# Optimization experiments

Measured on AMD Instinct MI355X. Metric: run time of the kernel, lower is better.

## Reference

```python
import jax, jax.numpy as jnp
import numpy as np

B, N, E, S, A, P, T = 512, 65536, 131072, 256, 512, 2, 64


def setup_inputs() -> dict:
    key = jax.random.key(0)
    ks = jax.random.split(key, 40)
    f32 = jnp.float32

    def g(i, shape, s=0.05):
        return jax.random.normal(ks[i], shape, f32) * s

    inp = {
        'nodes': jax.random.normal(ks[0], (N, S), f32),
        'edge_features': jax.random.normal(ks[1], (E, S), f32),
        'edge_source': jax.random.randint(ks[2], (E,), 0, N),
        'edge_dest': jax.random.randint(ks[3], (E,), 0, N),
        'node_owner': jax.random.randint(ks[4], (N,), 0, B),
        'running': jnp.ones((B,), bool),
        'ref_types': jax.random.randint(ks[5], (B,), 0, T),
        # decision aggregator (transform + sigmoid gate)
        'dec_t_W': g(6, (A, S)), 'dec_t_b': g(7, (A,)),
        'dec_g_W': g(8, (A, S)), 'dec_g_b': jnp.ones((A,), f32),
        # init aggregator
        'init_t_W': g(9, (A, S)), 'init_t_b': g(10, (A,)),
        'init_g_W': g(11, (A, S)), 'init_g_b': jnp.ones((A,), f32),
        # node type decision head + embedding
        'ntd_W': g(12, (T + 1, A)), 'ntd_b': g(13, (T + 1,)),
        'nte': g(14, (T, S), 1.0),
        # f_init
        'f1_W': g(15, (S, S)), 'f1_b': g(16, (S,)),
        'f2_W': g(17, (S, A)),
        # propagator params, stacked over P steps (message_size = 2S)
        'mn_W': g(18, (P, 2 * S, S)),
        'mf_W': g(19, (P, 2 * S, S)),
        'ml2_W': g(20, (P, 2 * S, 2 * S)), 'ml2_b': g(21, (P, 2 * S)),
        'gru_Wih': g(22, (P, 3 * S, 2 * S)), 'gru_Whh': g(23, (P, 3 * S, S)),
        'gru_bih': jnp.zeros((P, 3 * S), f32),
        'gru_bhh': jnp.concatenate(
            [jnp.ones((P, S), f32), jnp.zeros((P, 2 * S), f32)], axis=-1),
    }
    return inp


def _aggregate(nodes, fmask, tW, tb, gW, gb):
    # Aggregator.forward: sigmoid gate * linear transform, pooled per graph
    # via dense 0/1 owner-mask matmul (dropout=0 -> identity).
    gates = jax.nn.sigmoid(nodes @ gW.T + gb)
    data = nodes @ tW.T + tb
    return fmask @ (data * gates)  # [B, A]


def reference(nodes, edge_features, edge_source, edge_dest, node_owner,
              running, ref_types,
              dec_t_W, dec_t_b, dec_g_W, dec_g_b,
              init_t_W, init_t_b, init_g_W, init_g_b,
              ntd_W, ntd_b, nte, f1_W, f1_b, f2_W,
              mn_W, mf_W, ml2_W, ml2_b, gru_Wih, gru_Whh, gru_bih, gru_bhh):
    f32 = nodes.dtype
    fmask = (node_owner[None, :] == jnp.arange(B)[:, None]).astype(f32)  # [B,N]
    # Propagator._node_update_mask: owner_masks[running].sum(0) > 0
    upd = (fmask * running[:, None].astype(f32)).sum(0) > 0  # [N]

    for p in range(P):
        ef = edge_features @ mf_W[p].T                 # [E, 2S]
        nf = nodes @ mn_W[p].T                         # [N, 2S]
        msgs = nf[edge_source] + nf[edge_dest] + ef
        msgs = jnp.tanh(msgs) @ ml2_W[p].T + ml2_b[p]  # message_layer_2
        inputs = jnp.zeros((N, 2 * S), f32)
        inputs = inputs.at[edge_dest].add(msgs).at[edge_source].add(msgs)
        # torch GRUCell (gate order r, z, n)
        gi = inputs @ gru_Wih[p].T + gru_bih[p]
        gh = nodes @ gru_Whh[p].T + gru_bhh[p]
        ir, iz, inn = jnp.split(gi, 3, axis=-1)
        hr, hz, hn = jnp.split(gh, 3, axis=-1)
        r = jax.nn.sigmoid(ir + hr)
        z = jax.nn.sigmoid(iz + hz)
        n = jnp.tanh(inn + r * hn)
        new_nodes = (1.0 - z) * n + z * nodes
        nodes = jnp.where(upd[:, None], new_nodes, nodes)

    # node-type decision
    agg = _aggregate(nodes, fmask, dec_t_W, dec_t_b, dec_g_W, dec_g_b)
    logits = agg @ ntd_W.T + ntd_b                      # [B, T+1]

    # training path: remap_pad (no pad chars present) -> ref + 1
    sel = ref_types + 1                                  # in [1, T]
    logp = jax.nn.log_softmax(logits, axis=-1)
    per_ex = -logp[jnp.arange(B), sel]
    loss = jnp.where(running, per_ex, 0.0).mean()

    # new node features for running graphs
    emb = nte[sel - 1]                                   # [B, S]
    init_feats = _aggregate(nodes, fmask, init_t_W, init_t_b,
                            init_g_W, init_g_b)
    new_features = emb @ f1_W.T + f1_b + init_feats @ f2_W.T  # [B, S]
    return logits, new_features, loss
```

## Files before the change

kernel.cpp:

```cpp
#include <hip/hip_runtime.h>
#include <hip/hip_bf16.h>
#include <math.h>

#define BG 512
#define NN 65536
#define EE 131072
#define SD 256
#define AD 512
#define PP 2
#define TD 64

typedef __attribute__((ext_vector_type(8))) short sx8;
typedef __attribute__((ext_vector_type(4))) short sx4;
typedef __attribute__((ext_vector_type(4))) float fx4;

__device__ __forceinline__ float bs2f(short s) {
    union { unsigned u; float f; } x; x.u = ((unsigned)(unsigned short)s) << 16; return x.f;
}
__device__ __forceinline__ short f2bs(float f) {
    union { float f; unsigned u; } x; x.f = f;
    unsigned r = x.u + 0x7fffu + ((x.u >> 16) & 1u);
    return (short)(r >> 16);
}
__device__ __forceinline__ float fast_tanh(float x) {
    float xc = fminf(fmaxf(x, -15.f), 15.f);
    float e = __expf(2.f * xc);
    return __fdividef(e - 1.f, e + 1.f);
}
__device__ __forceinline__ float fast_sigm(float x) {
    float xc = fminf(fmaxf(x, -30.f), 30.f);
    float e = __expf(-xc);
    return __fdividef(1.f, 1.f + e);
}
__device__ __forceinline__ bool run_flag(const void* runv, int idx) {
    const unsigned char* r8 = (const unsigned char*)runv;
    const int* r32 = (const int*)runv;
    return (r8[idx] != 0) || (r32[idx] != 0);
}

__device__ __forceinline__ void gload16(const short* g, short* l) {
    __builtin_amdgcn_global_load_lds(
        (const __attribute__((address_space(1))) void*)g,
        (__attribute__((address_space(3))) void*)l, 16, 0, 0);
}

template<int EPI>
__launch_bounds__(256, 4)
__global__ void gemm_bt(const short* __restrict__ Abp,
                        const short* __restrict__ Wp, const float* __restrict__ bias,
                        short* __restrict__ Cout, float* __restrict__ Fout,
                        const float* __restrict__ bias2,
                        const short* __restrict__ nfp,
                        const int* __restrict__ esrc, const int* __restrict__ edst,
                        int K, int NC, int NT)
{
    __shared__ __align__(16) short sA[2 * 4096];
    __shared__ __align__(16) short sB[2 * 4096];
    const int t = threadIdx.x;
    const int lane = t & 63;
    const int w = t >> 6;

    const int nwg = gridDim.x;
    const int q = nwg >> 3;
    const int wg = (blockIdx.x & 7) * q + (blockIdx.x >> 3);
    const int mt = wg / NT;
    const int nt = wg - mt * NT;
    const int m0 = mt * 128;
    const int n0 = nt * 128;

    const int wm = (w >> 1) * 64;
    const int wn = (w & 1) * 64;
    const int lr = lane & 15;
    const int lg = lane >> 4;

    fx4 acc[4][4];
#pragma unroll
    for (int i = 0; i < 4; i++)
#pragma unroll
        for (int j = 0; j < 4; j++) { fx4 z = {0.f, 0.f, 0.f, 0.f}; acc[i][j] = z; }

    const int r = t >> 2;
    const int cblk = (t & 3) ^ ((r >> 1) & 3);
    const short* gA = Abp + (size_t)(m0 + r) * K + cblk * 8;
    const short* gB = Wp + (size_t)(n0 + r) * K + cblk * 8;
    const size_t rowskip = (size_t)64 * K;

    auto STAGE = [&](int b, int kk) {
        gload16(gA + kk,           sA + b * 4096 + w * 512);
        gload16(gA + kk + rowskip, sA + b * 4096 + 2048 + w * 512);
        gload16(gB + kk,           sB + b * 4096 + w * 512);
        gload16(gB + kk + rowskip, sB + b * 4096 + 2048 + w * 512);
    };

    STAGE(0, 0);
    __syncthreads();
    int buf = 0;
    const int xa = (lr >> 1) & 3;
    for (int kk = 0; kk < K; kk += 32) {
        if (kk + 32 < K) STAGE(buf ^ 1, kk + 32);
        const short* cA = sA + buf * 4096;
        const short* cB = sB + buf * 4096;
        sx8 af[4], bfr[4];
#pragma unroll
        for (int mi = 0; mi < 4; mi++)
            af[mi] = *(const sx8*)(cA + (wm + mi * 16 + lr) * 32 + (lg ^ xa) * 8);
#pragma unroll
        for (int ni = 0; ni < 4; ni++)
            bfr[ni] = *(const sx8*)(cB + (wn + ni * 16 + lr) * 32 + (lg ^ xa) * 8);
#pragma unroll
        for (int mi = 0; mi < 4; mi++)
#pragma unroll
            for (int ni = 0; ni < 4; ni++) {
                if (EPI == 4)
                    acc[mi][ni] = __builtin_amdgcn_mfma_f32_16x16x32_bf16(
                        af[mi], bfr[ni], acc[mi][ni], 0, 0, 0);
                else
                    acc[mi][ni] = __builtin_amdgcn_mfma_f32_16x16x32_bf16(
                        bfr[ni], af[mi], acc[mi][ni], 0, 0, 0);
            }
        __syncthreads();
        buf ^= 1;
    }

    if (EPI == 4) {
#pragma unroll
        for (int mi = 0; mi < 4; mi++) {
#pragma unroll
            for (int rg = 0; rg < 4; rg++) {
                const int m = m0 + wm + mi * 16 + lg * 4 + rg;
#pragma unroll
                for (int ni = 0; ni < 4; ni += 2) {
                    const int rc = (((n0 + wn + ni * 16) >> 5) << 4) + lr;
                    float dv = acc[mi][ni][rg] + bias[rc];
                    float gv = fast_sigm(acc[mi][ni + 1][rg] + bias2[rc]);
                    Fout[(size_t)m * 512 + rc] = dv * gv;
                }
            }
        }
    } else {
#pragma unroll
        for (int mi = 0; mi < 4; mi++) {
            const int m = m0 + wm + mi * 16 + lr;
            if (EPI == 2) {
                const int es = esrc[m], ed = edst[m];
                const short* ps = nfp + (size_t)es * NC + n0;
                const short* pd = nfp + (size_t)ed * NC + n0;
                short* co = Cout + (size_t)m * NC + n0;
#pragma unroll
                for (int ni = 0; ni < 4; ni++) {
                    const int nc = wn + ni * 16 + lg * 4;
                    sx4 a4 = *(const sx4*)(ps + nc);
                    sx4 b4 = *(const sx4*)(pd + nc);
                    sx4 o;
#pragma unroll
                    for (int rg = 0; rg < 4; rg++)
                        o[rg] = f2bs(fast_tanh(acc[mi][ni][rg]
                                               + bs2f(a4[rg]) + bs2f(b4[rg])));
                    *(sx4*)(co + nc) = o;
                }
            } else {
                short* co = Cout + (size_t)m * NC + n0;
#pragma unroll
                for (int ni = 0; ni < 4; ni++) {
                    const int nc = wn + ni * 16 + lg * 4;
                    fx4 vb = {0.f, 0.f, 0.f, 0.f};
                    if (bias) vb = *(const fx4*)(bias + n0 + nc);
                    sx4 o;
#pragma unroll
                    for (int rg = 0; rg < 4; rg++)
                        o[rg] = f2bs(acc[mi][ni][rg] + vb[rg]);
                    *(sx4*)(co + nc) = o;
                }
            }
        }
    }
}

__global__ void k_castw(const float* __restrict__ in, short* __restrict__ out)
{
    size_t i = ((size_t)blockIdx.x * 256 + threadIdx.x) * 4;
    fx4 v = *(const fx4*)(in + i);
    sx4 o;
#pragma unroll
    for (int u = 0; u < 4; u++) o[u] = f2bs(v[u]);
    *(sx4*)(out + i) = o;
}

__global__ void k_cast_pair(const float* __restrict__ tW, const float* __restrict__ gW,
                            short* __restrict__ out)
{
    size_t i = ((size_t)blockIdx.x * 256 + threadIdx.x) * 4;
    const int r2 = (int)(i >> 8);
    const int c = (int)(i & 255);
    const int src = ((r2 >> 5) << 4) | (r2 & 15);
    const float* W = ((r2 >> 4) & 1) ? gW : tW;
    fx4 v = *(const fx4*)(W + (size_t)src * 256 + c);
    sx4 o;
#pragma unroll
    for (int u = 0; u < 4; u++) o[u] = f2bs(v[u]);
    *(sx4*)(out + i) = o;
}

__global__ void k_count2(const int* __restrict__ a, const int* __restrict__ b,
                         int* __restrict__ deg, int n)
{
    int i = blockIdx.x * 256 + threadIdx.x;
    if (i < n) { atomicAdd(&deg[a[i]], 1); atomicAdd(&deg[b[i]], 1); }
}
__global__ void k_count1(const int* __restrict__ a, int* __restrict__ deg, int n)
{
    int i = blockIdx.x * 256 + threadIdx.x;
    if (i < n) atomicAdd(&deg[a[i]], 1);
}
__global__ void k_scan(const int* __restrict__ deg, int* __restrict__ offs, int n)
{
    __shared__ int part[256];
    const int t = threadIdx.x;
    const int chunk = n >> 8;
    const int base = t * chunk;
    int s = 0;
    for (int i = 0; i < chunk; i++) s += deg[base + i];
    part[t] = s;
    __syncthreads();
    for (int off = 1; off < 256; off <<= 1) {
        int v = (t >= off) ? part[t - off] : 0;
        __syncthreads();
        part[t] += v;
        __syncthreads();
    }
    int run = (t > 0) ? part[t - 1] : 0;
    for (int i = 0; i < chunk; i++) {
        offs[base + i] = run;
        run += deg[base + i];
    }
    if (t == 255) offs[n] = part[255];
}
__global__ void k_fill2(const int* __restrict__ a, const int* __restrict__ b,
                        const int* __restrict__ offs, int* __restrict__ cur,
                        int* __restrict__ elist, int n)
{
    int i = blockIdx.x * 256 + threadIdx.x;
    if (i < n) {
        int p = atomicAdd(&cur[a[i]], 1); elist[offs[a[i]] + p] = i;
        int q = atomicAdd(&cur[b[i]], 1); elist[offs[b[i]] + q] = i;
    }
}
__global__ void k_fill1(const int* __restrict__ own, const int* __restrict__ offs,
                        int* __restrict__ cur, int* __restrict__ nlist, int n)
{
    int i = blockIdx.x * 256 + threadIdx.x;
    if (i < n) {
        int p = atomicAdd(&cur[own[i]], 1); nlist[offs[own[i]] + p] = i;
    }
}

__global__ void k_edge_gather(const short* __restrict__ msgs, const int* __restrict__ offs,
                              const int* __restrict__ elist, short* __restrict__ inp)
{
    const int node = blockIdx.x * 4 + (threadIdx.x >> 6);
    const int c = (threadIdx.x & 63) * 8;
    const int s0 = offs[node], s1 = offs[node + 1];
    float acc[8] = {0.f, 0.f, 0.f, 0.f, 0.f, 0.f, 0.f, 0.f};
    for (int s = s0; s < s1; s++) {
        const int e = elist[s];
        sx8 v = *(const sx8*)(msgs + (size_t)e * 512 + c);
#pragma unroll
        for (int u = 0; u < 8; u++) acc[u] += bs2f(v[u]);
    }
    sx8 o;
#pragma unroll
    for (int u = 0; u < 8; u++) o[u] = f2bs(acc[u]);
    *(sx8*)(inp + (size_t)node * 512 + c) = o;
}

__global__ void k_owner_reduce(const float* __restrict__ gp, const int* __restrict__ offsB,
                               const int* __restrict__ nlist, float* __restrict__ agg)
{
    const int b = blockIdx.x, t = threadIdx.x;
    const int s0 = offsB[b], s1 = offsB[b + 1];
    float a0 = 0.f, a1 = 0.f;
    for (int s = s0; s < s1; s++) {
        const int n = nlist[s];
        float2 v = *(const float2*)(gp + (size_t)n * 512 + t * 2);
        a0 += v.x; a1 += v.y;
    }
    agg[(size_t)b * 512 + t * 2] = a0;
    agg[(size_t)b * 512 + t * 2 + 1] = a1;
}

__global__ void k_gru(const short* __restrict__ gi, const short* __restrict__ gh,
                      short* __restrict__ nodes,
                      const int* __restrict__ owner, const void* __restrict__ runv)
{
    const int n = blockIdx.x * 4 + (threadIdx.x >> 6);
    const int t = threadIdx.x & 63;
    const bool run = run_flag(runv, owner[n]);
    const size_t gb = (size_t)n * 768 + t * 4;
    sx4 vir = *(const sx4*)(gi + gb);
    sx4 viz = *(const sx4*)(gi + gb + 256);
    sx4 vin = *(const sx4*)(gi + gb + 512);
    sx4 whr = *(const sx4*)(gh + gb);
    sx4 whz = *(const sx4*)(gh + gb + 256);
    sx4 whn = *(const sx4*)(gh + gb + 512);
    const size_t nbase = (size_t)n * 256 + t * 4;
    sx4 old4 = *(const sx4*)(nodes + nbase);
    sx4 outb;
#pragma unroll
    for (int u = 0; u < 4; u++) {
        float old = bs2f(old4[u]);
        float rr = fast_sigm(bs2f(vir[u]) + bs2f(whr[u]));
        float zz = fast_sigm(bs2f(viz[u]) + bs2f(whz[u]));
        float nn = fast_tanh(bs2f(vin[u]) + rr * bs2f(whn[u]));
        float nv = (1.f - zz) * nn + zz * old;
        outb[u] = run ? f2bs(nv) : old4[u];
    }
    *(sx4*)(nodes + nbase) = outb;
}

__global__ void k_logits(const float* __restrict__ agg, const float* __restrict__ Wt,
                         const float* __restrict__ bt, float* __restrict__ logitsF,
                         float* __restrict__ outL)
{
    __shared__ float row[512];
    const int b = blockIdx.x, t = threadIdx.x;
    for (int k = t; k < 512; k += 128) row[k] = agg[(size_t)b * 512 + k];
    __syncthreads();
    if (t < TD + 1) {
        float acc = bt[t];
        const float* wr = Wt + (size_t)t * 512;
        for (int k = 0; k < 512; k++) acc += row[k] * wr[k];
        logitsF[b * (TD + 1) + t] = acc;
        outL[b * (TD + 1) + t] = acc;
    }
}

__global__ void k_loss(const float* __restrict__ logitsF, const int* __restrict__ reft,
                       const void* __restrict__ runv, float* __restrict__ outLoss)
{
    __shared__ float red[512];
    const int b = threadIdx.x;
    const float* lr = logitsF + b * (TD + 1);
    float mx = lr[0];
    for (int k = 1; k < TD + 1; k++) mx = fmaxf(mx, lr[k]);
    float se = 0.f;
    for (int k = 0; k < TD + 1; k++) se += expf(lr[k] - mx);
    const int sel = reft[b] + 1;
    float pe = logf(se) + mx - lr[sel];
    red[b] = run_flag(runv, b) ? pe : 0.f;
    __syncthreads();
    for (int s = 256; s > 0; s >>= 1) {
        if (b < s) red[b] += red[b + s];
        __syncthreads();
    }
    if (b == 0) outLoss[0] = red[0] / (float)BG;
}

__global__ void k_newfeat(const float* __restrict__ aggi, const float* __restrict__ nte,
                          const int* __restrict__ reft, const float* __restrict__ f1W,
                          const float* __restrict__ f1b, const float* __restrict__ f2W,
                          float* __restrict__ outNF)
{
    __shared__ float emb[256];
    __shared__ float ag[512];
    const int b = blockIdx.x, t = threadIdx.x;
    const int rt = reft[b];
    emb[t] = nte[(size_t)rt * 256 + t];
    ag[t] = aggi[(size_t)b * 512 + t];
    ag[t + 256] = aggi[(size_t)b * 512 + 256 + t];
    __syncthreads();
    float acc = f1b[t];
    const float* w1 = f1W + (size_t)t * 256;
    for (int k = 0; k < 256; k++) acc += emb[k] * w1[k];
    const float* w2 = f2W + (size_t)t * 512;
    for (int a = 0; a < 512; a++) acc += ag[a] * w2[a];
    outNF[(size_t)b * 256 + t] = acc;
}

extern "C" void kernel_launch(void* const* d_in, const int* in_sizes, int n_in,
                              void* d_out, int out_size, void* d_ws, size_t ws_size,
                              hipStream_t stream)
{
    (void)in_sizes; (void)n_in; (void)out_size;
    const float* in_nodes = (const float*)d_in[0];
    const float* in_ef    = (const float*)d_in[1];
    const int*   e_src    = (const int*)d_in[2];
    const int*   e_dst    = (const int*)d_in[3];
    const int*   owner    = (const int*)d_in[4];
    const void*  running  = d_in[5];
    const int*   reft     = (const int*)d_in[6];
    const float* dec_tW = (const float*)d_in[7];
    const float* dec_tb = (const float*)d_in[8];
    const float* dec_gW = (const float*)d_in[9];
    const float* dec_gb = (const float*)d_in[10];
    const float* init_tW = (const float*)d_in[11];
    const float* init_tb = (const float*)d_in[12];
    const float* init_gW = (const float*)d_in[13];
    const float* init_gb = (const float*)d_in[14];
    const float* ntdW = (const float*)d_in[15];
    const float* ntdb = (const float*)d_in[16];
    const float* nte  = (const float*)d_in[17];
    const float* f1W  = (const float*)d_in[18];
    const float* f1b  = (const float*)d_in[19];
    const float* f2W  = (const float*)d_in[20];
    const float* mnW  = (const float*)d_in[21];
    const float* mfW  = (const float*)d_in[22];
    const float* ml2W = (const float*)d_in[23];
    const float* ml2b = (const float*)d_in[24];
    const float* Wih  = (const float*)d_in[25];
    const float* Whh  = (const float*)d_in[26];
    const float* bih  = (const float*)d_in[27];
    const float* bhh  = (const float*)d_in[28];

    float* outL    = (float*)d_out;
    float* outNF   = outL + BG * (TD + 1);
    float* outLoss = outNF + BG * SD;

    size_t off = 0;
    auto take = [&](size_t bytes) -> void* {
        void* p = (char*)d_ws + off;
        off += (bytes + 255) & ~(size_t)255;
        return p;
    };
    short* nodes_bf  = (short*)take((size_t)NN * SD * 2);
    short* ef_bf     = (short*)take((size_t)EE * SD * 2);
    short* bufC      = (short*)take((size_t)NN * 512 * 2);
    short* bufD      = (short*)take((size_t)EE * 512 * 2);
    short* bufM      = (short*)take((size_t)EE * 512 * 2);
    short* bufI      = (short*)take((size_t)NN * 512 * 2);
    float* aggD      = (float*)take((size_t)BG * AD * 4);
    float* aggI      = (float*)take((size_t)BG * AD * 4);
    float* logitsF   = (float*)take((size_t)BG * (TD + 1) * 4);
    short* mnWb  = (short*)take((size_t)PP * 512 * 256 * 2);
    short* mfWb  = (short*)take((size_t)PP * 512 * 256 * 2);
    short* ml2Wb = (short*)take((size_t)PP * 512 * 512 * 2);
    short* WihB  = (short*)take((size_t)PP * 768 * 512 * 2);
    short* WhhB  = (short*)take((size_t)PP * 768 * 256 * 2);
    short* W2dec = (short*)take((size_t)1024 * 256 * 2);
    short* W2ini = (short*)take((size_t)1024 * 256 * 2);
    int* deg_e = (int*)take((size_t)NN * 4);
    int* offs_e = (int*)take((size_t)(NN + 1) * 4);
    int* cur_e = (int*)take((size_t)NN * 4);
    int* elist = (int*)take((size_t)2 * EE * 4);
    int* degB = (int*)take((size_t)BG * 4);
    int* offsB = (int*)take((size_t)(BG + 1) * 4);
    int* curB = (int*)take((size_t)BG * 4);
    int* nlist = (int*)take((size_t)NN * 4);
    if (off > ws_size) return;

    short* gi = bufD;
    short* gh = bufM;
    float* gp = (float*)bufM;

    k_castw<<<NN * SD / 1024, 256, 0, stream>>>(in_nodes, nodes_bf);
    k_castw<<<EE * SD / 1024, 256, 0, stream>>>(in_ef, ef_bf);
    k_castw<<<PP * 512 * 256 / 1024, 256, 0, stream>>>(mnW, mnWb);
    k_castw<<<PP * 512 * 256 / 1024, 256, 0, stream>>>(mfW, mfWb);
    k_castw<<<PP * 512 * 512 / 1024, 256, 0, stream>>>(ml2W, ml2Wb);
    k_castw<<<PP * 768 * 512 / 1024, 256, 0, stream>>>(Wih, WihB);
    k_castw<<<PP * 768 * 256 / 1024, 256, 0, stream>>>(Whh, WhhB);
    k_cast_pair<<<1024 * 256 / 1024, 256, 0, stream>>>(dec_tW, dec_gW, W2dec);
    k_cast_pair<<<1024 * 256 / 1024, 256, 0, stream>>>(init_tW, init_gW, W2ini);

    hipMemsetAsync(deg_e, 0, (size_t)NN * 4, stream);
    hipMemsetAsync(cur_e, 0, (size_t)NN * 4, stream);
    hipMemsetAsync(degB, 0, (size_t)BG * 4, stream);
    hipMemsetAsync(curB, 0, (size_t)BG * 4, stream);
    k_count2<<<(EE + 255) / 256, 256, 0, stream>>>(e_src, e_dst, deg_e, EE);
    k_scan<<<1, 256, 0, stream>>>(deg_e, offs_e, NN);
    k_fill2<<<(EE + 255) / 256, 256, 0, stream>>>(e_src, e_dst, offs_e, cur_e, elist, EE);
    k_count1<<<(NN + 255) / 256, 256, 0, stream>>>(owner, degB, NN);
    k_scan<<<1, 256, 0, stream>>>(degB, offsB, BG);
    k_fill1<<<(NN + 255) / 256, 256, 0, stream>>>(owner, offsB, curB, nlist, NN);

    for (int p = 0; p < PP; p++) {
        gemm_bt<0><<<NN / 128 * 4, 256, 0, stream>>>(
            nodes_bf, mnWb + (size_t)p * 512 * 256, nullptr, bufC,
            nullptr, nullptr, nullptr, nullptr, nullptr, 256, 512, 4);
        gemm_bt<2><<<EE / 128 * 4, 256, 0, stream>>>(
            ef_bf, mfWb + (size_t)p * 512 * 256, nullptr, bufD,
            nullptr, nullptr, bufC, e_src, e_dst, 256, 512, 4);
        gemm_bt<0><<<EE / 128 * 4, 256, 0, stream>>>(
            bufD, ml2Wb + (size_t)p * 512 * 512, ml2b + (size_t)p * 512,
            bufM, nullptr, nullptr, nullptr, nullptr, nullptr, 512, 512, 4);
        k_edge_gather<<<NN / 4, 256, 0, stream>>>(bufM, offs_e, elist, bufI);
        gemm_bt<0><<<NN / 128 * 6, 256, 0, stream>>>(
            bufI, WihB + (size_t)p * 768 * 512, bih + (size_t)p * 768, gi,
            nullptr, nullptr, nullptr, nullptr, nullptr, 512, 768, 6);
        gemm_bt<0><<<NN / 128 * 6, 256, 0, stream>>>(
            nodes_bf, WhhB + (size_t)p * 768 * 256, bhh + (size_t)p * 768, gh,
            nullptr, nullptr, nullptr, nullptr, nullptr, 256, 768, 6);
        k_gru<<<NN / 4, 256, 0, stream>>>(gi, gh, nodes_bf, owner, running);
    }

    gemm_bt<4><<<NN / 128 * 8, 256, 0, stream>>>(
        nodes_bf, W2dec, dec_tb, nullptr, gp, dec_gb,
        nullptr, nullptr, nullptr, 256, 1024, 8);
    k_owner_reduce<<<BG, 256, 0, stream>>>(gp, offsB, nlist, aggD);
    gemm_bt<4><<<NN / 128 * 8, 256, 0, stream>>>(
        nodes_bf, W2ini, init_tb, nullptr, gp, init_gb,
        nullptr, nullptr, nullptr, 256, 1024, 8);
    k_owner_reduce<<<BG, 256, 0, stream>>>(gp, offsB, nlist, aggI);

    k_logits<<<BG, 128, 0, stream>>>(aggD, ntdW, ntdb, logitsF, outL);
    k_loss<<<1, 512, 0, stream>>>(logitsF, reft, running, outLoss);
    k_newfeat<<<BG, 256, 0, stream>>>(aggI, nte, reft, f1W, f1b, f2W, outNF);
}
```

Before: 1.886 ms.

## Triple-buffer GEMM k-loop with explicit vmcnt waits and merge aggregator GEMMs

The GEMM main loop moves from double to triple LDS buffering, prefetching two k-steps ahead and replacing __syncthreads with raw barriers plus explicit vmcnt waits, so global-to-LDS loads overlap more MFMA work. Edge source/dest indices for the EPI=2 epilogue are loaded before the loop. The two aggregator GEMMs (decision and init) are merged into one launch over a concatenated 2048-wide weight, with the epilogue routing each column tile to its own output. The larger LDS footprint lowers launch bounds to 3 blocks per CU, which may reduce occupancy.

```diff
diff --git a/kernel.cpp b/kernel.cpp
--- a/kernel.cpp
+++ b/kernel.cpp
@@ -45,17 +45,18 @@
 }
 
 template<int EPI>
-__launch_bounds__(256, 4)
-__global__ void gemm_bt(const short* __restrict__ Abp,
-                        const short* __restrict__ Wp, const float* __restrict__ bias,
+__launch_bounds__(256, 3)
+__global__ void gemm_bt(const short* __restrict__ Abp, const short* __restrict__ Wp,
+                        const float* __restrict__ bias, const float* __restrict__ bias2,
                         short* __restrict__ Cout, float* __restrict__ Fout,
-                        const float* __restrict__ bias2,
+                        float* __restrict__ FoutB,
+                        const float* __restrict__ biasB, const float* __restrict__ biasB2,
                         const short* __restrict__ nfp,
                         const int* __restrict__ esrc, const int* __restrict__ edst,
-                        int K, int NC, int NT)
-{
-    __shared__ __align__(16) short sA[2 * 4096];
-    __shared__ __align__(16) short sB[2 * 4096];
+                        int K, int NC, int NT, int nsplit)
+{
+    __shared__ __align__(16) short sA[3 * 4096];
+    __shared__ __align__(16) short sB[3 * 4096];
     const int t = threadIdx.x;
     const int lane = t & 63;
     const int w = t >> 6;
@@ -93,13 +94,33 @@
     };
 
     STAGE(0, 0);
-    __syncthreads();
-    int buf = 0;
+    STAGE(1, 32);
+
+    int es[4], ed[4];
+    if (EPI == 2) {
+#pragma unroll
+        for (int mi = 0; mi < 4; mi++) {
+            const int m = m0 + wm + mi * 16 + lr;
+            es[mi] = esrc[m]; ed[mi] = edst[m];
+        }
+    }
+
+    const int T = K >> 5;
+    int cur = 0;
     const int xa = (lr >> 1) & 3;
-    for (int kk = 0; kk < K; kk += 32) {
-        if (kk + 32 < K) STAGE(buf ^ 1, kk + 32);
-        const short* cA = sA + buf * 4096;
-        const short* cB = sB + buf * 4096;
+    for (int i = 0; i < T; i++) {
+        __builtin_amdgcn_s_barrier();
+        if (i + 2 < T) {
+            STAGE((cur >= 1) ? cur - 1 : cur + 2, (i + 2) << 5);
+            asm volatile("s_waitcnt vmcnt(8)" ::: "memory");
+        } else if (i + 1 < T) {
+            asm volatile("s_waitcnt vmcnt(4)" ::: "memory");
+        } else {
+            asm volatile("s_waitcnt vmcnt(0)" ::: "memory");
+        }
+        __builtin_amdgcn_s_barrier();
+        const short* cA = sA + cur * 4096;
+        const short* cB = sB + cur * 4096;
         sx8 af[4], bfr[4];
 #pragma unroll
         for (int mi = 0; mi < 4; mi++)
@@ -118,11 +139,15 @@
                     acc[mi][ni] = __builtin_amdgcn_mfma_f32_16x16x32_bf16(
                         bfr[ni], af[mi], acc[mi][ni], 0, 0, 0);
             }
-        __syncthreads();
-        buf ^= 1;
+        cur = (cur == 2) ? 0 : cur + 1;
     }
 
     if (EPI == 4) {
+        const bool useB = (n0 >= nsplit);
+        float* fo = useB ? FoutB : Fout;
+        const float* tb = useB ? biasB : bias;
+        const float* gb = useB ? biasB2 : bias2;
+        const int ln0 = useB ? (n0 - nsplit) : n0;
 #pragma unroll
         for (int mi = 0; mi < 4; mi++) {
 #pragma unroll
@@ -130,10 +155,10 @@
                 const int m = m0 + wm + mi * 16 + lg * 4 + rg;
 #pragma unroll
                 for (int ni = 0; ni < 4; ni += 2) {
-                    const int rc = (((n0 + wn + ni * 16) >> 5) << 4) + lr;
-                    float dv = acc[mi][ni][rg] + bias[rc];
-                    float gv = fast_sigm(acc[mi][ni + 1][rg] + bias2[rc]);
-                    Fout[(size_t)m * 512 + rc] = dv * gv;
+                    const int rc = (((ln0 + wn + ni * 16) >> 5) << 4) + lr;
+                    float dv = acc[mi][ni][rg] + tb[rc];
+                    float gv = fast_sigm(acc[mi][ni + 1][rg] + gb[rc]);
+                    fo[(size_t)m * 512 + rc] = dv * gv;
                 }
             }
         }
@@ -142,9 +167,8 @@
         for (int mi = 0; mi < 4; mi++) {
             const int m = m0 + wm + mi * 16 + lr;
             if (EPI == 2) {
-                const int es = esrc[m], ed = edst[m];
-                const short* ps = nfp + (size_t)es * NC + n0;
-                const short* pd = nfp + (size_t)ed * NC + n0;
+                const short* ps = nfp + (size_t)es[mi] * NC + n0;
+                const short* pd = nfp + (size_t)ed[mi] * NC + n0;
                 short* co = Cout + (size_t)m * NC + n0;
 #pragma unroll
                 for (int ni = 0; ni < 4; ni++) {
@@ -435,8 +459,7 @@
     short* ml2Wb = (short*)take((size_t)PP * 512 * 512 * 2);
     short* WihB  = (short*)take((size_t)PP * 768 * 512 * 2);
     short* WhhB  = (short*)take((size_t)PP * 768 * 256 * 2);
-    short* W2dec = (short*)take((size_t)1024 * 256 * 2);
-    short* W2ini = (short*)take((size_t)1024 * 256 * 2);
+    short* W4agg = (short*)take((size_t)2048 * 256 * 2);
     int* deg_e = (int*)take((size_t)NN * 4);
     int* offs_e = (int*)take((size_t)(NN + 1) * 4);
     int* cur_e = (int*)take((size_t)NN * 4);
@@ -449,7 +472,8 @@
 
     short* gi = bufD;
     short* gh = bufM;
-    float* gp = (float*)bufM;
+    float* gpD = (float*)bufM;
+    float* gpI = (float*)bufD;
 
     k_castw<<<NN * SD / 1024, 256, 0, stream>>>(in_nodes, nodes_bf);
     k_castw<<<EE * SD / 1024, 256, 0, stream>>>(in_ef, ef_bf);
@@ -458,8 +482,9 @@
     k_castw<<<PP * 512 * 512 / 1024, 256, 0, stream>>>(ml2W, ml2Wb);
     k_castw<<<PP * 768 * 512 / 1024, 256, 0, stream>>>(Wih, WihB);
     k_castw<<<PP * 768 * 256 / 1024, 256, 0, stream>>>(Whh, WhhB);
-    k_cast_pair<<<1024 * 256 / 1024, 256, 0, stream>>>(dec_tW, dec_gW, W2dec);
-    k_cast_pair<<<1024 * 256 / 1024, 256, 0, stream>>>(init_tW, init_gW, W2ini);
+    k_cast_pair<<<1024 * 256 / 1024, 256, 0, stream>>>(dec_tW, dec_gW, W4agg);
+    k_cast_pair<<<1024 * 256 / 1024, 256, 0, stream>>>(init_tW, init_gW,
+                                                       W4agg + 1024 * 256);
 
     hipMemsetAsync(deg_e, 0, (size_t)NN * 4, stream);
     hipMemsetAsync(cur_e, 0, (size_t)NN * 4, stream);
@@ -474,32 +499,35 @@
 
     for (int p = 0; p < PP; p++) {
         gemm_bt<0><<<NN / 128 * 4, 256, 0, stream>>>(
-            nodes_bf, mnWb + (size_t)p * 512 * 256, nullptr, bufC,
-            nullptr, nullptr, nullptr, nullptr, nullptr, 256, 512, 4);
+            nodes_bf, mnWb + (size_t)p * 512 * 256, nullptr, nullptr, bufC,
+            nullptr, nullptr, nullptr, nullptr, nullptr, nullptr, nullptr,
+            256, 512, 4, 0);
         gemm_bt<2><<<EE / 128 * 4, 256, 0, stream>>>(
-            ef_bf, mfWb + (size_t)p * 512 * 256, nullptr, bufD,
-            nullptr, nullptr, bufC, e_src, e_dst, 256, 512, 4);
+            ef_bf, mfWb + (size_t)p * 512 * 256, nullptr, nullptr, bufD,
+            nullptr, nullptr, nullptr, nullptr, bufC, e_src, e_dst,
+            256, 512, 4, 0);
         gemm_bt<0><<<EE / 128 * 4, 256, 0, stream>>>(
-            bufD, ml2Wb + (size_t)p * 512 * 512, ml2b + (size_t)p * 512,
-            bufM, nullptr, nullptr, nullptr, nullptr, nullptr, 512, 512, 4);
+            bufD, ml2Wb + (size_t)p * 512 * 512, ml2b + (size_t)p * 512, nullptr,
+            bufM, nullptr, nullptr, nullptr, nullptr, nullptr, nullptr, nullptr,
+            512, 512, 4, 0);
         k_edge_gather<<<NN / 4, 256, 0, stream>>>(bufM, offs_e, elist, bufI);
         gemm_bt<0><<<NN / 128 * 6, 256, 0, stream>>>(
-            bufI, WihB + (size_t)p * 768 * 512, bih + (size_t)p * 768, gi,
-            nullptr, nullptr, nullptr, nullptr, nullptr, 512, 768, 6);
+            bufI, WihB + (size_t)p * 768 * 512, bih + (size_t)p * 768, nullptr,
+            gi, nullptr, nullptr, nullptr, nullptr, nullptr, nullptr, nullptr,
+            512, 768, 6, 0);
         gemm_bt<0><<<NN / 128 * 6, 256, 0, stream>>>(
-            nodes_bf, WhhB + (size_t)p * 768 * 256, bhh + (size_t)p * 768, gh,
-            nullptr, nullptr, nullptr, nullptr, nullptr, 256, 768, 6);
+            nodes_bf, WhhB + (size_t)p * 768 * 256, bhh + (size_t)p * 768, nullptr,
+            gh, nullptr, nullptr, nullptr, nullptr, nullptr, nullptr, nullptr,
+            256, 768, 6, 0);
         k_gru<<<NN / 4, 256, 0, stream>>>(gi, gh, nodes_bf, owner, running);
     }
 
-    gemm_bt<4><<<NN / 128 * 8, 256, 0, stream>>>(
-        nodes_bf, W2dec, dec_tb, nullptr, gp, dec_gb,
-        nullptr, nullptr, nullptr, 256, 1024, 8);
-    k_owner_reduce<<<BG, 256, 0, stream>>>(gp, offsB, nlist, aggD);
-    gemm_bt<4><<<NN / 128 * 8, 256, 0, stream>>>(
-        nodes_bf, W2ini, init_tb, nullptr, gp, init_gb,
-        nullptr, nullptr, nullptr, 256, 1024, 8);
-    k_owner_reduce<<<BG, 256, 0, stream>>>(gp, offsB, nlist, aggI);
+    gemm_bt<4><<<NN / 128 * 16, 256, 0, stream>>>(
+        nodes_bf, W4agg, dec_tb, dec_gb, nullptr, gpD, gpI,
+        init_tb, init_gb, nullptr, nullptr, nullptr,
+        256, 2048, 16, 1024);
+    k_owner_reduce<<<BG, 256, 0, stream>>>(gpD, offsB, nlist, aggD);
+    k_owner_reduce<<<BG, 256, 0, stream>>>(gpI, offsB, nlist, aggI);
 
     k_logits<<<BG, 128, 0, stream>>>(aggD, ntdW, ntdb, logitsF, outL);
     k_loss<<<1, 512, 0, stream>>>(logitsF, reft, running, outLoss);
```

Result: slower. 1.983 ms (+5.1%).
